# Performance work log

Measured on AMD Instinct MI355X. Metric: run time of the kernel, lower is better.

Reference implementation:

```python
import jax, jax.numpy as jnp
import numpy as np
import math

N_HEADS = 16
LN_EPS = 1e-5


def _layernorm(x, scale, bias):
    mu = jnp.mean(x, axis=-1, keepdims=True)
    var = jnp.var(x, axis=-1, keepdims=True)
    return (x - mu) * jax.lax.rsqrt(var + LN_EPS) * scale + bias


def _pos_encoding(seq_len, d_model, dtype):
    pos = jnp.arange(seq_len, dtype=jnp.float32)[:, None]
    div = jnp.exp(jnp.arange(0, d_model, 2, dtype=jnp.float32) * (-math.log(10000.0) / d_model))
    pe = jnp.zeros((seq_len, d_model), dtype=jnp.float32)
    pe = pe.at[:, 0::2].set(jnp.sin(pos * div))
    pe = pe.at[:, 1::2].set(jnp.cos(pos * div))
    return pe.astype(dtype)


def setup_inputs() -> dict:
    key = jax.random.key(0)
    ks = jax.random.split(key, 8)
    B, S, V, D, L = 2, 1024, 32000, 1024, 6
    F = 4 * D
    sc = 0.02
    return {
        "tokens": jax.random.randint(ks[0], (B, S), 0, V, dtype=jnp.int32),
        "token_emb": jax.random.normal(ks[1], (V, D), jnp.float32) * sc,
        "Wqkv": jax.random.normal(ks[2], (L, D, 3 * D), jnp.float32) * sc,
        "Wout": jax.random.normal(ks[3], (L, D, D), jnp.float32) * sc,
        "ln1_s": jnp.ones((L, D), jnp.float32),
        "ln1_b": jnp.zeros((L, D), jnp.float32),
        "W1": jax.random.normal(ks[4], (L, D, F), jnp.float32) * sc,
        "b1": jnp.zeros((L, F), jnp.float32),
        "W2": jax.random.normal(ks[5], (L, F, D), jnp.float32) * sc,
        "b2": jnp.zeros((L, D), jnp.float32),
        "ln2_s": jnp.ones((L, D), jnp.float32),
        "ln2_b": jnp.zeros((L, D), jnp.float32),
        "lnf_s": jnp.ones((D,), jnp.float32),
        "lnf_b": jnp.zeros((D,), jnp.float32),
        "Whead": jax.random.normal(ks[6], (D, V), jnp.float32) * sc,
        "bhead": jnp.zeros((V,), jnp.float32),
    }


def _forward(tokens, token_emb, Wqkv, Wout, ln1_s, ln1_b, W1, b1, W2, b2,
             ln2_s, ln2_b, lnf_s, lnf_b, Whead, bhead):
    B, S = tokens.shape
    D = token_emb.shape[1]
    L = Wqkv.shape[0]
    H = N_HEADS
    dk = D // H

    x = token_emb[tokens] + _pos_encoding(S, D, token_emb.dtype)  # [B,S,D]
    causal = jnp.tril(jnp.ones((S, S), dtype=bool))
    neg_inf = jnp.finfo(x.dtype).min

    for l in range(L):
        # --- attention sublayer ---
        h = _layernorm(x, ln1_s[l], ln1_b[l])
        qkv = (h @ Wqkv[l]).reshape(B, S, 3, H, dk)
        q, k, v = jnp.moveaxis(qkv, 2, 0)  # each [B,S,H,dk]
        scores = jnp.einsum('bqhd,bkhd->bhqk', q, k) / math.sqrt(dk)
        scores = jnp.where(causal, scores, neg_inf)
        attn = jax.nn.softmax(scores, axis=-1)  # [B,H,S,S]
        o = jnp.einsum('bhqk,bkhd->bqhd', attn, v).reshape(B, S, D)
        x = x + o @ Wout[l]
        # --- FFN sublayer ---
        h2 = _layernorm(x, ln2_s[l], ln2_b[l])
        x = x + jax.nn.gelu(h2 @ W1[l] + b1[l], approximate=False) @ W2[l] + b2[l]

    x = _layernorm(x, lnf_s, lnf_b)
    return x @ Whead + bhead  # [B,S,V]


def reference(tokens, token_emb, Wqkv, Wout, ln1_s, ln1_b, W1, b1, W2, b2,
              ln2_s, ln2_b, lnf_s, lnf_b, Whead, bhead):
    return _forward(tokens, token_emb, Wqkv, Wout, ln1_s, ln1_b, W1, b1, W2, b2,
                    ln2_s, ln2_b, lnf_s, lnf_b, Whead, bhead)
```

## Files before the change

kernel.cpp:

```cpp
#include <hip/hip_runtime.h>
#include <hip/hip_bf16.h>
#include <math.h>

typedef __bf16 bf16;
typedef __bf16 bf16x4 __attribute__((ext_vector_type(4)));
typedef __bf16 bf16x8 __attribute__((ext_vector_type(8)));
typedef float f32x4 __attribute__((ext_vector_type(4)));

#define GL_AS(p) ((const __attribute__((address_space(1))) void*)(p))
#define LDS_AS(p) ((__attribute__((address_space(3))) void*)(p))

__device__ inline void xcd_remap(int& bm, int& bn, int NBM, int NBN)
{
    const int nwg = NBM * NBN;
    const int flat = bm + NBM * bn;
    const int q = nwg >> 3, r = nwg & 7;
    const int x = flat & 7, i = flat >> 3;
    const int f2 = ((x < r) ? x * (q + 1) : r * (q + 1) + (x - r) * q) + i;
    bm = f2 % NBM;
    bn = f2 / NBM;
}

struct TSeg {
    const float* in; bf16* out; int R, C, nTilesC, tilesPerZ, nTiles;
};

__global__ __launch_bounds__(256) void transpose_all_k(
    TSeg s0, TSeg s1, TSeg s2, TSeg s3, TSeg s4)
{
    int t = blockIdx.x;
    TSeg s;
    if (t < s0.nTiles) s = s0;
    else { t -= s0.nTiles;
    if (t < s1.nTiles) s = s1;
    else { t -= s1.nTiles;
    if (t < s2.nTiles) s = s2;
    else { t -= s2.nTiles;
    if (t < s3.nTiles) s = s3;
    else { t -= s3.nTiles; s = s4; }}}}

    const int z   = t / s.tilesPerZ;
    const int rem = t - z * s.tilesPerZ;
    const int cx  = rem % s.nTilesC, ry = rem / s.nTilesC;

    __shared__ float tl[32][33];
    const int c0 = cx * 32, r0 = ry * 32;
    const size_t zoff = (size_t)z * s.R * s.C;
    const float* inb = s.in + zoff;
    bf16* outb = s.out + zoff;
    const int tx = threadIdx.x, ty = threadIdx.y;
#pragma unroll
    for (int i = 0; i < 32; i += 8)
        tl[ty + i][tx] = inb[(size_t)(r0 + ty + i) * s.C + c0 + tx];
    __syncthreads();
#pragma unroll
    for (int i = 0; i < 32; i += 8)
        outb[(size_t)(c0 + ty + i) * s.R + r0 + tx] = (bf16)tl[tx][ty + i];
}

__global__ __launch_bounds__(256) void embed_k(
    const int* __restrict__ tok, const float* __restrict__ emb,
    float* __restrict__ x)
{
    const int D = 1024;
    const int row = blockIdx.x;
    const int s = row & 1023;
    const int t = tok[row];
    const int d0 = threadIdx.x * 4;
    const float c = 9.210340371976184f / 512.0f;
    const float div0 = expf(-(float)(d0 >> 1) * c);
    const float div1 = expf(-(float)((d0 >> 1) + 1) * c);
    const float a0 = (float)s * div0, a1 = (float)s * div1;
    const f32x4 e = *(const f32x4*)(emb + (size_t)t * D + d0);
    f32x4 o;
    o[0] = e[0] + sinf(a0);
    o[1] = e[1] + cosf(a0);
    o[2] = e[2] + sinf(a1);
    o[3] = e[3] + cosf(a1);
    *(f32x4*)(x + (size_t)row * D + d0) = o;
}

__global__ __launch_bounds__(256) void layernorm_k(
    const float* __restrict__ x, const float* __restrict__ sc,
    const float* __restrict__ bi, bf16* __restrict__ out)
{
    const int D = 1024;
    const int row = blockIdx.x;
    const int d0 = threadIdx.x * 4;
    const f32x4 v = *(const f32x4*)(x + (size_t)row * D + d0);
    float s = v[0] + v[1] + v[2] + v[3];
    float q = v[0] * v[0] + v[1] * v[1] + v[2] * v[2] + v[3] * v[3];
#pragma unroll
    for (int o = 32; o; o >>= 1) { s += __shfl_xor(s, o); q += __shfl_xor(q, o); }
    __shared__ float ls[4], lq[4];
    const int w = threadIdx.x >> 6;
    if ((threadIdx.x & 63) == 0) { ls[w] = s; lq[w] = q; }
    __syncthreads();
    const float S = ls[0] + ls[1] + ls[2] + ls[3];
    const float Q = lq[0] + lq[1] + lq[2] + lq[3];
    const float mu = S * (1.0f / D);
    const float var = Q * (1.0f / D) - mu * mu;
    const float rstd = rsqrtf(var + 1e-5f);
    const f32x4 sc4 = *(const f32x4*)(sc + d0);
    const f32x4 bi4 = *(const f32x4*)(bi + d0);
    bf16x4 o4;
#pragma unroll
    for (int i = 0; i < 4; ++i) o4[i] = (bf16)((v[i] - mu) * rstd * sc4[i] + bi4[i]);
    *(bf16x4*)(out + (size_t)row * D + d0) = o4;
}

template <int EPI, int SK = 1>
__global__ __launch_bounds__(256, 2) void gemm_bt_k(
    const bf16* __restrict__ A, const bf16* __restrict__ Bt,
    float* __restrict__ Cf, bf16* __restrict__ Cb, bf16* __restrict__ Cb2,
    const float* __restrict__ bias, int M, int N, int K)
{
    __shared__ __align__(16) bf16 Al[128 * 64];
    __shared__ __align__(16) bf16 Bl[128 * 64];
    const int tid = threadIdx.x;
    const int l = tid & 63;
    const int wbase = tid & 192;
    const int wr = (tid >> 7) & 1, wc = (tid >> 6) & 1;
    int bm = blockIdx.x, bn = blockIdx.y;
    xcd_remap(bm, bn, gridDim.x, gridDim.y);
    const int kz = blockIdx.z;
    const int Kc = K / SK;

    f32x4 acc[4][4];
#pragma unroll
    for (int i = 0; i < 4; ++i)
#pragma unroll
        for (int j = 0; j < 4; ++j) acc[i][j] = (f32x4){0.f, 0.f, 0.f, 0.f};

    const bf16* Abase = A + (size_t)bm * 128 * K + (size_t)kz * Kc;
    const bf16* Bbase = Bt + (size_t)bn * 128 * K + (size_t)kz * Kc;

    for (int k0 = 0; k0 < Kc; k0 += 64) {
#pragma unroll
        for (int i = 0; i < 4; ++i) {
            const int c = i * 256 + tid;
            const int row = c >> 3, slot = c & 7;
            const int col = ((slot ^ (row & 7)) << 3);
            __builtin_amdgcn_global_load_lds(
                GL_AS(Abase + (size_t)row * K + k0 + col),
                LDS_AS(Al + (i * 256 + wbase) * 8), 16, 0, 0);
        }
#pragma unroll
        for (int i = 0; i < 4; ++i) {
            const int c = i * 256 + tid;
            const int row = c >> 3, slot = c & 7;
            const int col = ((slot ^ (row & 7)) << 3);
            __builtin_amdgcn_global_load_lds(
                GL_AS(Bbase + (size_t)row * K + k0 + col),
                LDS_AS(Bl + (i * 256 + wbase) * 8), 16, 0, 0);
        }
        __syncthreads();

#pragma unroll
        for (int ks = 0; ks < 2; ++ks) {
            bf16x8 af[4], bfr[4];
            const int kb = ks * 64 + ((l >> 4) << 4);
#pragma unroll
            for (int mi = 0; mi < 4; ++mi) {
                const int r = wr * 64 + mi * 16 + (l & 15);
                af[mi] = *(const bf16x8*)((const char*)Al + r * 128 + (kb ^ ((r & 7) << 4)));
            }
#pragma unroll
            for (int ni = 0; ni < 4; ++ni) {
                const int r = wc * 64 + ni * 16 + (l & 15);
                bfr[ni] = *(const bf16x8*)((const char*)Bl + r * 128 + (kb ^ ((r & 7) << 4)));
            }
#pragma unroll
            for (int mi = 0; mi < 4; ++mi)
#pragma unroll
                for (int ni = 0; ni < 4; ++ni)
                    acc[mi][ni] = __builtin_amdgcn_mfma_f32_16x16x32_bf16(
                        af[mi], bfr[ni], acc[mi][ni], 0, 0, 0);
        }
        __syncthreads();
    }

    const int colb = bn * 128 + wc * 64;
    const int rowb = bm * 128 + wr * 64 + ((l >> 4) << 2);
#pragma unroll
    for (int mi = 0; mi < 4; ++mi) {
#pragma unroll
        for (int ni = 0; ni < 4; ++ni) {
            const int col = colb + ni * 16 + (l & 15);
            if constexpr (EPI == 5) {
                const int row0 = rowb + mi * 16;
                if (col < 2048) {
#pragma unroll
                    for (int j = 0; j < 4; ++j)
                        Cb[(size_t)(row0 + j) * N + col] = (bf16)acc[mi][ni][j];
                } else {
                    bf16x4 v4;
#pragma unroll
                    for (int j = 0; j < 4; ++j) v4[j] = (bf16)acc[mi][ni][j];
                    *(bf16x4*)&Cb2[((size_t)(row0 >> 3) * 1024 + (col - 2048)) * 8 + (row0 & 7)] = v4;
                }
            } else {
#pragma unroll
                for (int j = 0; j < 4; ++j) {
                    const int row = rowb + mi * 16 + j;
                    const float v = acc[mi][ni][j];
                    if constexpr (EPI == 0) {
                        Cb[(size_t)row * N + col] = (bf16)v;
                    } else if constexpr (EPI == 1) {
                        if constexpr (SK > 1) atomicAdd(&Cf[(size_t)row * N + col], v);
                        else                  Cf[(size_t)row * N + col] += v;
                    } else if constexpr (EPI == 2) {
                        const float u = v + bias[col];
                        const float g = 0.5f * u * (1.0f + erff(u * 0.70710678118654752f));
                        Cb[(size_t)row * N + col] = (bf16)g;
                    } else if constexpr (EPI == 3) {
                        const float add = (SK == 1 || kz == 0) ? v + bias[col] : v;
                        if constexpr (SK > 1) atomicAdd(&Cf[(size_t)row * N + col], add);
                        else                  Cf[(size_t)row * N + col] += add;
                    } else if constexpr (EPI == 4) {
                        Cf[(size_t)row * N + col] = v + bias[col];
                    }
                }
            }
        }
    }
}

__global__ __launch_bounds__(512, 2) void gemm256_bias_k(
    const bf16* __restrict__ A, const bf16* __restrict__ Bt,
    float* __restrict__ Cf, const float* __restrict__ bias,
    int M, int N, int K)
{
    __shared__ __align__(16) bf16 Al[2][256 * 64];
    __shared__ __align__(16) bf16 Bl[2][256 * 64];
    const int tid = threadIdx.x;
    const int l = tid & 63;
    const int wid = tid >> 6;
    const int wm = wid >> 2, wn = wid & 3;
    const int g = l >> 4, lc = l & 15;
    int bm = blockIdx.x, bn = blockIdx.y;
    xcd_remap(bm, bn, gridDim.x, gridDim.y);

    const bf16* Ab = A + (size_t)bm * 256 * K;
    const bf16* Bb = Bt + (size_t)bn * 256 * K;
    const int NT = K >> 6;

    f32x4 acc[8][4];
#pragma unroll
    for (int i = 0; i < 8; ++i)
#pragma unroll
        for (int j = 0; j < 4; ++j) acc[i][j] = (f32x4){0.f, 0.f, 0.f, 0.f};

    auto stageA = [&](int t, int mh) {
        bf16* dst = Al[t & 1] + mh * 8192;
#pragma unroll
        for (int ld = 0; ld < 2; ++ld) {
            const int c = ld * 512 + tid;
            const int r = c >> 3, slot = c & 7;
            const int col = ((slot ^ (r & 7)) << 3);
            __builtin_amdgcn_global_load_lds(
                GL_AS(Ab + (size_t)(mh * 128 + r) * K + t * 64 + col),
                LDS_AS(dst + (ld * 512 + (tid & 448)) * 8), 16, 0, 0);
        }
    };
    auto stageB = [&](int t, int nh) {
        bf16* dst = Bl[t & 1] + nh * 8192;
#pragma unroll
        for (int ld = 0; ld < 2; ++ld) {
            const int c = ld * 512 + tid;
            const int r = c >> 3, slot = c & 7;
            const int col = ((slot ^ (r & 7)) << 3);
            __builtin_amdgcn_global_load_lds(
                GL_AS(Bb + (size_t)(nh * 128 + r) * K + t * 64 + col),
                LDS_AS(dst + (ld * 512 + (tid & 448)) * 8), 16, 0, 0);
        }
    };
    auto ldA = [&](bf16x8 (&a)[4][2], int mh, int p) {
#pragma unroll
        for (int i = 0; i < 4; ++i) {
            const int r = wm * 128 + mh * 64 + i * 16 + lc;
            const char* base = (const char*)Al[p] + r * 128;
#pragma unroll
            for (int ks = 0; ks < 2; ++ks)
                a[i][ks] = *(const bf16x8*)(base + ((ks * 64 + g * 16) ^ ((r & 7) << 4)));
        }
    };
    auto ldB = [&](bf16x8 (&b)[2][2], int nh, int p) {
#pragma unroll
        for (int i = 0; i < 2; ++i) {
            const int r = wn * 64 + nh * 32 + i * 16 + lc;
            const char* base = (const char*)Bl[p] + r * 128;
#pragma unroll
            for (int ks = 0; ks < 2; ++ks)
                b[i][ks] = *(const bf16x8*)(base + ((ks * 64 + g * 16) ^ ((r & 7) << 4)));
        }
    };
    auto mm = [&](bf16x8 (&a)[4][2], bf16x8 (&b)[2][2], int mh, int nh) {
        __builtin_amdgcn_s_setprio(1);
#pragma unroll
        for (int i = 0; i < 4; ++i)
#pragma unroll
            for (int jn = 0; jn < 2; ++jn) {
                f32x4 ac = acc[mh * 4 + i][nh * 2 + jn];
                ac = __builtin_amdgcn_mfma_f32_16x16x32_bf16(a[i][0], b[jn][0], ac, 0, 0, 0);
                ac = __builtin_amdgcn_mfma_f32_16x16x32_bf16(a[i][1], b[jn][1], ac, 0, 0, 0);
                acc[mh * 4 + i][nh * 2 + jn] = ac;
            }
        __builtin_amdgcn_s_setprio(0);
    };

    stageB(0, 0); stageB(0, 1); stageA(0, 0); stageA(0, 1);
    if (NT > 1) { stageB(1, 0); stageB(1, 1); }
    asm volatile("s_waitcnt vmcnt(4)" ::: "memory");
    __builtin_amdgcn_s_barrier();

    for (int t = 0; t < NT; ++t) {
        const int p = t & 1;
        bf16x8 a[4][2], b0[2][2], b1[2][2];
        ldA(a, 0, p); ldB(b0, 0, p);
        if (t + 1 < NT) stageA(t + 1, 0);
        __builtin_amdgcn_s_barrier();
        mm(a, b0, 0, 0);
        __builtin_amdgcn_s_barrier();
        ldB(b1, 1, p);
        if (t + 1 < NT) stageA(t + 1, 1);
        __builtin_amdgcn_s_barrier();
        mm(a, b1, 0, 1);
        __builtin_amdgcn_s_barrier();
        ldA(a, 1, p);
        if (t + 2 < NT) stageB(t + 2, 0);
        __builtin_amdgcn_s_barrier();
        mm(a, b1, 1, 1);
        __builtin_amdgcn_s_barrier();
        if (t + 2 < NT) stageB(t + 2, 1);
        asm volatile("s_waitcnt vmcnt(4)" ::: "memory");
        __builtin_amdgcn_s_barrier();
        mm(a, b0, 1, 0);
        __builtin_amdgcn_s_barrier();
    }

    const int colb = bn * 256 + wn * 64;
    const int rowb = bm * 256 + wm * 128 + g * 4;
#pragma unroll
    for (int mi = 0; mi < 8; ++mi) {
#pragma unroll
        for (int ni = 0; ni < 4; ++ni) {
            const int col = colb + ni * 16 + lc;
#pragma unroll
            for (int j = 0; j < 4; ++j) {
                const int row = rowb + mi * 16 + j;
                Cf[(size_t)row * N + col] = acc[mi][ni][j] + bias[col];
            }
        }
    }
}

__global__ __launch_bounds__(256) void attn_mfma_k(
    const bf16* __restrict__ qkv, const bf16* __restrict__ vt,
    bf16* __restrict__ o)
{
    __shared__ __align__(16) bf16 Kl[2][32 * 64];
    __shared__ __align__(16) bf16 Vl[2][64 * 32];
    __shared__ __align__(16) bf16 Pl[4][16][88];

    const int tid = threadIdx.x;
    const int w = tid >> 6, l = tid & 63;
    const int g = l >> 4, lc = l & 15;
    const int qt = blockIdx.x & 15;
    const int bh = blockIdx.x >> 4;
    const int h = bh & 15, b = bh >> 4;
    const int q0 = qt * 64;
    const int qw = q0 + w * 16;
    const int diag = qw >> 5;
    const int NT = (q0 >> 5) + 2;

    const bf16* qbase = qkv + (size_t)b * 1024 * 3072 + h * 64;
    const bf16* kbase = qbase + 1024;
    const bf16* vbase = vt + (size_t)b * 128 * 8192 + h * 64 * 8;

    bf16x8 af0, af1;
    {
        const bf16* qp = qbase + (size_t)(qw + lc) * 3072 + g * 8;
        af0 = *(const bf16x8*)qp;
        af1 = *(const bf16x8*)(qp + 32);
    }

    f32x4 acc[4];
#pragma unroll
    for (int dt = 0; dt < 4; ++dt) acc[dt] = (f32x4){0.f, 0.f, 0.f, 0.f};
    f32x4 m  = (f32x4){-1e30f, -1e30f, -1e30f, -1e30f};
    f32x4 ls = (f32x4){0.f, 0.f, 0.f, 0.f};

    auto stage = [&](int t) {
        const int k0 = t * 32;
        const int buf = t & 1;
        {
            const int row = tid >> 3;
            const int d = (((tid & 7) ^ (row & 7)) << 3);
            __builtin_amdgcn_global_load_lds(
                GL_AS(kbase + (size_t)(k0 + row) * 3072 + d),
                LDS_AS(Kl[buf] + (tid & 192) * 8), 16, 0, 0);
        }
        {
            const int row = tid >> 2;
            const int so = (tid & 3) ^ ((tid >> 3) & 3);
            __builtin_amdgcn_global_load_lds(
                GL_AS(vbase + (size_t)((k0 >> 3) + so) * 8192 + row * 8),
                LDS_AS(Vl[buf] + (tid & 192) * 8), 16, 0, 0);
        }
    };

    auto compute = [&](int t, bool MASKED) {
        const char* KT = (const char*)Kl[t & 1];
        const char* VT = (const char*)Vl[t & 1];
        const int k0 = t * 32;

        const int r0 = lc, r1 = 16 + lc;
        const bf16x8 kf00 = *(const bf16x8*)(KT + r0 * 128 + 16 * (g       ^ (r0 & 7)));
        const bf16x8 kf01 = *(const bf16x8*)(KT + r0 * 128 + 16 * ((4 + g) ^ (r0 & 7)));
        const bf16x8 kf10 = *(const bf16x8*)(KT + r1 * 128 + 16 * (g       ^ (r1 & 7)));
        const bf16x8 kf11 = *(const bf16x8*)(KT + r1 * 128 + 16 * ((4 + g) ^ (r1 & 7)));

        f32x4 s0 = (f32x4){0.f, 0.f, 0.f, 0.f};
        f32x4 s1 = (f32x4){0.f, 0.f, 0.f, 0.f};
        s0 = __builtin_amdgcn_mfma_f32_16x16x32_bf16(af0, kf00, s0, 0, 0, 0);
        s0 = __builtin_amdgcn_mfma_f32_16x16x32_bf16(af1, kf01, s0, 0, 0, 0);
        s1 = __builtin_amdgcn_mfma_f32_16x16x32_bf16(af0, kf10, s1, 0, 0, 0);
        s1 = __builtin_amdgcn_mfma_f32_16x16x32_bf16(af1, kf11, s1, 0, 0, 0);

#pragma unroll
        for (int j = 0; j < 4; ++j) {
            if (MASKED) {
                const int row = qw + 4 * g + j;
                s0[j] = (k0 + lc <= row)      ? s0[j] * 0.125f : -1e30f;
                s1[j] = (k0 + 16 + lc <= row) ? s1[j] * 0.125f : -1e30f;
            } else {
                s0[j] *= 0.125f;
                s1[j] *= 0.125f;
            }
        }

        f32x4 tmx;
#pragma unroll
        for (int j = 0; j < 4; ++j) tmx[j] = fmaxf(s0[j], s1[j]);
#pragma unroll
        for (int off = 8; off; off >>= 1)
#pragma unroll
            for (int j = 0; j < 4; ++j) tmx[j] = fmaxf(tmx[j], __shfl_xor(tmx[j], off));

        f32x4 sc, p0, p1;
#pragma unroll
        for (int j = 0; j < 4; ++j) {
            const float mn = fmaxf(m[j], tmx[j]);
            sc[j] = __expf(m[j] - mn);
            p0[j] = __expf(s0[j] - mn);
            p1[j] = __expf(s1[j] - mn);
            m[j] = mn;
            ls[j] = ls[j] * sc[j] + p0[j] + p1[j];
        }
#pragma unroll
        for (int dt = 0; dt < 4; ++dt)
#pragma unroll
            for (int j = 0; j < 4; ++j) acc[dt][j] *= sc[j];

#pragma unroll
        for (int j = 0; j < 4; ++j) {
            const int r = 4 * g + j;
            const bf16 h0 = (bf16)p0[j];
            const bf16 h1 = (bf16)p1[j];
            Pl[w][r][lc]      = h0;
            Pl[w][r][16 + lc] = h1;
            Pl[w][r][48 + lc] = (bf16)(p0[j] - (float)h0);
            Pl[w][r][64 + lc] = (bf16)(p1[j] - (float)h1);
        }
        const bf16x8 pah = *(const bf16x8*)&Pl[w][lc][g * 8];
        const bf16x8 pal = *(const bf16x8*)&Pl[w][lc][48 + g * 8];

#pragma unroll
        for (int dt = 0; dt < 4; ++dt) {
            const int vr = dt * 16 + lc;
            const bf16x8 vf = *(const bf16x8*)(VT + vr * 64 + 16 * (g ^ ((vr >> 1) & 3)));
            acc[dt] = __builtin_amdgcn_mfma_f32_16x16x32_bf16(pah, vf, acc[dt], 0, 0, 0);
            acc[dt] = __builtin_amdgcn_mfma_f32_16x16x32_bf16(pal, vf, acc[dt], 0, 0, 0);
        }
    };

    stage(0);
    __syncthreads();
    for (int t = 0; t < NT; ++t) {
        if (t + 1 < NT) stage(t + 1);
        if (t <= diag) compute(t, t == diag);
        __syncthreads();
    }

    f32x4 inv;
#pragma unroll
    for (int j = 0; j < 4; ++j) {
        float s = ls[j];
#pragma unroll
        for (int off = 8; off; off >>= 1) s += __shfl_xor(s, off);
        inv[j] = 1.0f / s;
    }
    bf16* op = o + (size_t)(b * 1024 + qw) * 1024 + h * 64;
#pragma unroll
    for (int dt = 0; dt < 4; ++dt)
#pragma unroll
        for (int j = 0; j < 4; ++j)
            op[(size_t)(4 * g + j) * 1024 + dt * 16 + lc] = (bf16)(acc[dt][j] * inv[j]);
}

extern "C" void kernel_launch(void* const* d_in, const int* in_sizes, int n_in,
                              void* d_out, int out_size, void* d_ws, size_t ws_size,
                              hipStream_t stream)
{
    const int B = 2, S = 1024, D = 1024, L = 6, F = 4096, V = 32000, H = 16;
    const int M = B * S;

    const int*   tokens    = (const int*)  d_in[0];
    const float* token_emb = (const float*)d_in[1];
    const float* Wqkv      = (const float*)d_in[2];
    const float* Wout      = (const float*)d_in[3];
    const float* ln1_s     = (const float*)d_in[4];
    const float* ln1_b     = (const float*)d_in[5];
    const float* W1        = (const float*)d_in[6];
    const float* b1        = (const float*)d_in[7];
    const float* W2        = (const float*)d_in[8];
    const float* b2        = (const float*)d_in[9];
    const float* ln2_s     = (const float*)d_in[10];
    const float* ln2_b     = (const float*)d_in[11];
    const float* lnf_s     = (const float*)d_in[12];
    const float* lnf_b     = (const float*)d_in[13];
    const float* Whead     = (const float*)d_in[14];
    const float* bhead     = (const float*)d_in[15];
    float* out = (float*)d_out;

    char* w = (char*)d_ws;
    size_t off = 0;
    auto alloc = [&](size_t n) { char* p = w + off; off += (n + 255) & ~(size_t)255; return p; };
    bf16* WqkvT  = (bf16*)alloc((size_t)L * 3 * D * D * 2);
    bf16* WoutT  = (bf16*)alloc((size_t)L * D * D * 2);
    bf16* W1T    = (bf16*)alloc((size_t)L * F * D * 2);
    bf16* W2T    = (bf16*)alloc((size_t)L * D * F * 2);
    bf16* WheadT = (bf16*)alloc((size_t)V * D * 2);
    float* x     = (float*)alloc((size_t)M * D * 4);
    bf16* h      = (bf16*)alloc((size_t)M * D * 2);
    bf16* qkv    = (bf16*)alloc((size_t)M * 3 * D * 2);
    bf16* ob     = (bf16*)alloc((size_t)M * D * 2);
    bf16* mid    = (bf16*)alloc((size_t)M * F * 2);
    bf16* vt     = mid;

    TSeg s0{Wqkv,  WqkvT,  D, 3 * D, 3 * D / 32, (3 * D / 32) * (D / 32), (3 * D / 32) * (D / 32) * L};
    TSeg s1{Wout,  WoutT,  D, D,     D / 32,     (D / 32) * (D / 32),     (D / 32) * (D / 32) * L};
    TSeg s2{W1,    W1T,    D, F,     F / 32,     (F / 32) * (D / 32),     (F / 32) * (D / 32) * L};
    TSeg s3{W2,    W2T,    F, D,     D / 32,     (D / 32) * (F / 32),     (D / 32) * (F / 32) * L};
    TSeg s4{Whead, WheadT, D, V,     V / 32,     (V / 32) * (D / 32),     (V / 32) * (D / 32)};
    const int totTiles = s0.nTiles + s1.nTiles + s2.nTiles + s3.nTiles + s4.nTiles;
    transpose_all_k<<<totTiles, dim3(32, 8), 0, stream>>>(s0, s1, s2, s3, s4);

    embed_k<<<M, 256, 0, stream>>>(tokens, token_emb, x);

    for (int lyr = 0; lyr < L; ++lyr) {
        layernorm_k<<<M, 256, 0, stream>>>(x, ln1_s + lyr * D, ln1_b + lyr * D, h);
        gemm_bt_k<5><<<dim3(M / 128, 3 * D / 128), 256, 0, stream>>>(
            h, WqkvT + (size_t)lyr * 3 * D * D, nullptr, qkv, vt, nullptr, M, 3 * D, D);
        attn_mfma_k<<<B * H * S / 64, 256, 0, stream>>>(qkv, vt, ob);
        gemm_bt_k<1, 4><<<dim3(M / 128, D / 128, 4), 256, 0, stream>>>(
            ob, WoutT + (size_t)lyr * D * D, x, nullptr, nullptr, nullptr, M, D, D);
        layernorm_k<<<M, 256, 0, stream>>>(x, ln2_s + lyr * D, ln2_b + lyr * D, h);
        gemm_bt_k<2><<<dim3(M / 128, F / 128), 256, 0, stream>>>(
            h, W1T + (size_t)lyr * F * D, nullptr, mid, nullptr, b1 + lyr * F, M, F, D);
        gemm_bt_k<3, 4><<<dim3(M / 128, D / 128, 4), 256, 0, stream>>>(
            mid, W2T + (size_t)lyr * D * F, x, nullptr, nullptr, b2 + lyr * D, M, D, F);
    }
    layernorm_k<<<M, 256, 0, stream>>>(x, lnf_s, lnf_b, h);
    gemm256_bias_k<<<dim3(M / 256, V / 256), 512, 0, stream>>>(
        h, WheadT, out, bhead, M, V, D);
}
```

Before: 1.585 ms.

## Widen attention KV tiles to 64 and add explicit LDS waits in GEMM phases

The attention kernel now processes 64 keys per iteration instead of 32. This halves the number of loop iterations, barriers and online-softmax rescales per query tile, but every wave now computes its masked diagonal tile in full even where part of it is masked out. The GEMM mainloop also gets phase syncs that pair each barrier with sched_barrier and lgkmcnt(0) waits, and drains vmcnt fully on the final iterations. These extra waits add stricter ordering, and the larger LDS buffers and per-thread register state may reduce occupancy.

Result: faster. 1.511 ms (-4.7%).

```diff
diff --git a/kernel.cpp b/kernel.cpp
--- a/kernel.cpp
+++ b/kernel.cpp
@@ -308,6 +308,12 @@
             }
         __builtin_amdgcn_s_setprio(0);
     };
+    auto phase_sync = [&]() {
+        __builtin_amdgcn_sched_barrier(0);
+        __builtin_amdgcn_s_barrier();
+        asm volatile("s_waitcnt lgkmcnt(0)" ::: "memory");
+        __builtin_amdgcn_sched_barrier(0);
+    };
 
     stageB(0, 0); stageB(0, 1); stageA(0, 0); stageA(0, 1);
     if (NT > 1) { stageB(1, 0); stageB(1, 1); }
@@ -319,22 +325,26 @@
         bf16x8 a[4][2], b0[2][2], b1[2][2];
         ldA(a, 0, p); ldB(b0, 0, p);
         if (t + 1 < NT) stageA(t + 1, 0);
-        __builtin_amdgcn_s_barrier();
+        phase_sync();
         mm(a, b0, 0, 0);
         __builtin_amdgcn_s_barrier();
         ldB(b1, 1, p);
         if (t + 1 < NT) stageA(t + 1, 1);
-        __builtin_amdgcn_s_barrier();
+        phase_sync();
         mm(a, b1, 0, 1);
         __builtin_amdgcn_s_barrier();
         ldA(a, 1, p);
         if (t + 2 < NT) stageB(t + 2, 0);
-        __builtin_amdgcn_s_barrier();
+        phase_sync();
         mm(a, b1, 1, 1);
         __builtin_amdgcn_s_barrier();
         if (t + 2 < NT) stageB(t + 2, 1);
-        asm volatile("s_waitcnt vmcnt(4)" ::: "memory");
+        __builtin_amdgcn_sched_barrier(0);
+        if (t + 2 < NT) asm volatile("s_waitcnt vmcnt(4)" ::: "memory");
+        else            asm volatile("s_waitcnt vmcnt(0)" ::: "memory");
         __builtin_amdgcn_s_barrier();
+        asm volatile("s_waitcnt lgkmcnt(0)" ::: "memory");
+        __builtin_amdgcn_sched_barrier(0);
         mm(a, b0, 1, 0);
         __builtin_amdgcn_s_barrier();
     }
@@ -359,9 +369,9 @@
     const bf16* __restrict__ qkv, const bf16* __restrict__ vt,
     bf16* __restrict__ o)
 {
-    __shared__ __align__(16) bf16 Kl[2][32 * 64];
-    __shared__ __align__(16) bf16 Vl[2][64 * 32];
-    __shared__ __align__(16) bf16 Pl[4][16][88];
+    __shared__ __align__(16) bf16 Kl[2][64 * 64];
+    __shared__ __align__(16) bf16 Vl[2][64 * 64];
+    __shared__ __align__(16) bf16 Pl[4][16][136];
 
     const int tid = threadIdx.x;
     const int w = tid >> 6, l = tid & 63;
@@ -371,12 +381,11 @@
     const int h = bh & 15, b = bh >> 4;
     const int q0 = qt * 64;
     const int qw = q0 + w * 16;
-    const int diag = qw >> 5;
-    const int NT = (q0 >> 5) + 2;
+    const int NT = qt + 1;
 
     const bf16* qbase = qkv + (size_t)b * 1024 * 3072 + h * 64;
     const bf16* kbase = qbase + 1024;
-    const bf16* vbase = vt + (size_t)b * 128 * 8192 + h * 64 * 8;
+    const bf16* vbase = vt + (size_t)b * 128 * 8192 + h * 512;
 
     bf16x8 af0, af1;
     {
@@ -392,72 +401,81 @@
     f32x4 ls = (f32x4){0.f, 0.f, 0.f, 0.f};
 
     auto stage = [&](int t) {
-        const int k0 = t * 32;
+        const int k0 = t * 64;
         const int buf = t & 1;
-        {
-            const int row = tid >> 3;
-            const int d = (((tid & 7) ^ (row & 7)) << 3);
+#pragma unroll
+        for (int ld = 0; ld < 2; ++ld) {
+            const int c = ld * 256 + tid;
+            const int row = c >> 3;
+            const int d = (((c & 7) ^ (row & 7)) << 3);
             __builtin_amdgcn_global_load_lds(
                 GL_AS(kbase + (size_t)(k0 + row) * 3072 + d),
-                LDS_AS(Kl[buf] + (tid & 192) * 8), 16, 0, 0);
-        }
-        {
-            const int row = tid >> 2;
-            const int so = (tid & 3) ^ ((tid >> 3) & 3);
+                LDS_AS(Kl[buf] + (ld * 256 + (tid & 192)) * 8), 16, 0, 0);
+        }
+#pragma unroll
+        for (int ld = 0; ld < 2; ++ld) {
+            const int c = ld * 256 + tid;
+            const int row = c >> 3;
+            const int so = (c & 7) ^ (row & 7);
             __builtin_amdgcn_global_load_lds(
                 GL_AS(vbase + (size_t)((k0 >> 3) + so) * 8192 + row * 8),
-                LDS_AS(Vl[buf] + (tid & 192) * 8), 16, 0, 0);
+                LDS_AS(Vl[buf] + (ld * 256 + (tid & 192)) * 8), 16, 0, 0);
         }
     };
 
     auto compute = [&](int t, bool MASKED) {
         const char* KT = (const char*)Kl[t & 1];
         const char* VT = (const char*)Vl[t & 1];
-        const int k0 = t * 32;
-
-        const int r0 = lc, r1 = 16 + lc;
-        const bf16x8 kf00 = *(const bf16x8*)(KT + r0 * 128 + 16 * (g       ^ (r0 & 7)));
-        const bf16x8 kf01 = *(const bf16x8*)(KT + r0 * 128 + 16 * ((4 + g) ^ (r0 & 7)));
-        const bf16x8 kf10 = *(const bf16x8*)(KT + r1 * 128 + 16 * (g       ^ (r1 & 7)));
-        const bf16x8 kf11 = *(const bf16x8*)(KT + r1 * 128 + 16 * ((4 + g) ^ (r1 & 7)));
-
-        f32x4 s0 = (f32x4){0.f, 0.f, 0.f, 0.f};
-        f32x4 s1 = (f32x4){0.f, 0.f, 0.f, 0.f};
-        s0 = __builtin_amdgcn_mfma_f32_16x16x32_bf16(af0, kf00, s0, 0, 0, 0);
-        s0 = __builtin_amdgcn_mfma_f32_16x16x32_bf16(af1, kf01, s0, 0, 0, 0);
-        s1 = __builtin_amdgcn_mfma_f32_16x16x32_bf16(af0, kf10, s1, 0, 0, 0);
-        s1 = __builtin_amdgcn_mfma_f32_16x16x32_bf16(af1, kf11, s1, 0, 0, 0);
-
+        const int k0 = t * 64;
+
+        f32x4 s[4];
+#pragma unroll
+        for (int kt = 0; kt < 4; ++kt) {
+            const int r = kt * 16 + lc;
+            const bf16x8 kf0 = *(const bf16x8*)(KT + r * 128 + ((g * 16)      ^ ((r & 7) << 4)));
+            const bf16x8 kf1 = *(const bf16x8*)(KT + r * 128 + ((64 + g * 16) ^ ((r & 7) << 4)));
+            f32x4 sv = (f32x4){0.f, 0.f, 0.f, 0.f};
+            sv = __builtin_amdgcn_mfma_f32_16x16x32_bf16(af0, kf0, sv, 0, 0, 0);
+            sv = __builtin_amdgcn_mfma_f32_16x16x32_bf16(af1, kf1, sv, 0, 0, 0);
+            s[kt] = sv;
+        }
+
+#pragma unroll
+        for (int kt = 0; kt < 4; ++kt)
+#pragma unroll
+            for (int j = 0; j < 4; ++j) {
+                if (MASKED) {
+                    const int row = qw + 4 * g + j;
+                    s[kt][j] = (k0 + kt * 16 + lc <= row) ? s[kt][j] * 0.125f : -1e30f;
+                } else {
+                    s[kt][j] *= 0.125f;
+                }
+            }
+
+        f32x4 tm;
+#pragma unroll
+        for (int j = 0; j < 4; ++j)
+            tm[j] = fmaxf(fmaxf(s[0][j], s[1][j]), fmaxf(s[2][j], s[3][j]));
+#pragma unroll
+        for (int off = 8; off; off >>= 1)
+#pragma unroll
+            for (int j = 0; j < 4; ++j) tm[j] = fmaxf(tm[j], __shfl_xor(tm[j], off));
+
+        f32x4 sc;
 #pragma unroll
         for (int j = 0; j < 4; ++j) {
-            if (MASKED) {
-                const int row = qw + 4 * g + j;
-                s0[j] = (k0 + lc <= row)      ? s0[j] * 0.125f : -1e30f;
-                s1[j] = (k0 + 16 + lc <= row) ? s1[j] * 0.125f : -1e30f;
-            } else {
-                s0[j] *= 0.125f;
-                s1[j] *= 0.125f;
-            }
-        }
-
-        f32x4 tmx;
-#pragma unroll
-        for (int j = 0; j < 4; ++j) tmx[j] = fmaxf(s0[j], s1[j]);
-#pragma unroll
-        for (int off = 8; off; off >>= 1)
-#pragma unroll
-            for (int j = 0; j < 4; ++j) tmx[j] = fmaxf(tmx[j], __shfl_xor(tmx[j], off));
-
-        f32x4 sc, p0, p1;
-#pragma unroll
-        for (int j = 0; j < 4; ++j) {
-            const float mn = fmaxf(m[j], tmx[j]);
+            const float mn = fmaxf(m[j], tm[j]);
             sc[j] = __expf(m[j] - mn);
-            p0[j] = __expf(s0[j] - mn);
-            p1[j] = __expf(s1[j] - mn);
             m[j] = mn;
-            ls[j] = ls[j] * sc[j] + p0[j] + p1[j];
-        }
+        }
+        f32x4 p[4];
+#pragma unroll
+        for (int kt = 0; kt < 4; ++kt)
+#pragma unroll
+            for (int j = 0; j < 4; ++j) p[kt][j] = __expf(s[kt][j] - m[j]);
+#pragma unroll
+        for (int j = 0; j < 4; ++j)
+            ls[j] = ls[j] * sc[j] + ((p[0][j] + p[1][j]) + (p[2][j] + p[3][j]));
 #pragma unroll
         for (int dt = 0; dt < 4; ++dt)
 #pragma unroll
@@ -466,22 +484,31 @@
 #pragma unroll
         for (int j = 0; j < 4; ++j) {
             const int r = 4 * g + j;
-            const bf16 h0 = (bf16)p0[j];
-            const bf16 h1 = (bf16)p1[j];
-            Pl[w][r][lc]      = h0;
-            Pl[w][r][16 + lc] = h1;
-            Pl[w][r][48 + lc] = (bf16)(p0[j] - (float)h0);
-            Pl[w][r][64 + lc] = (bf16)(p1[j] - (float)h1);
-        }
-        const bf16x8 pah = *(const bf16x8*)&Pl[w][lc][g * 8];
-        const bf16x8 pal = *(const bf16x8*)&Pl[w][lc][48 + g * 8];
+#pragma unroll
+            for (int kt = 0; kt < 4; ++kt) {
+                const bf16 hi = (bf16)p[kt][j];
+                Pl[w][r][kt * 16 + lc]      = hi;
+                Pl[w][r][72 + kt * 16 + lc] = (bf16)(p[kt][j] - (float)hi);
+            }
+        }
+        bf16x8 pah[2], pal[2];
+#pragma unroll
+        for (int ks = 0; ks < 2; ++ks) {
+            pah[ks] = *(const bf16x8*)&Pl[w][lc][ks * 32 + g * 8];
+            pal[ks] = *(const bf16x8*)&Pl[w][lc][72 + ks * 32 + g * 8];
+        }
 
 #pragma unroll
         for (int dt = 0; dt < 4; ++dt) {
-            const int vr = dt * 16 + lc;
-            const bf16x8 vf = *(const bf16x8*)(VT + vr * 64 + 16 * (g ^ ((vr >> 1) & 3)));
-            acc[dt] = __builtin_amdgcn_mfma_f32_16x16x32_bf16(pah, vf, acc[dt], 0, 0, 0);
-            acc[dt] = __builtin_amdgcn_mfma_f32_16x16x32_bf16(pal, vf, acc[dt], 0, 0, 0);
+            const int r = dt * 16 + lc;
+            const bf16x8 vf0 = *(const bf16x8*)(VT + r * 128 + ((g * 16)      ^ ((r & 7) << 4)));
+            const bf16x8 vf1 = *(const bf16x8*)(VT + r * 128 + ((64 + g * 16) ^ ((r & 7) << 4)));
+            f32x4 a = acc[dt];
+            a = __builtin_amdgcn_mfma_f32_16x16x32_bf16(pah[0], vf0, a, 0, 0, 0);
+            a = __builtin_amdgcn_mfma_f32_16x16x32_bf16(pah[1], vf1, a, 0, 0, 0);
+            a = __builtin_amdgcn_mfma_f32_16x16x32_bf16(pal[0], vf0, a, 0, 0, 0);
+            a = __builtin_amdgcn_mfma_f32_16x16x32_bf16(pal[1], vf1, a, 0, 0, 0);
+            acc[dt] = a;
         }
     };
 
@@ -489,7 +516,7 @@
     __syncthreads();
     for (int t = 0; t < NT; ++t) {
         if (t + 1 < NT) stage(t + 1);
-        if (t <= diag) compute(t, t == diag);
+        compute(t, t == NT - 1);
         __syncthreads();
     }
 
```
